# Kernel tuning notes

Hardware: AMD Instinct MI355X
Metric: run time of the kernel (lower is better)

## Reference

```python
import jax, jax.numpy as jnp
import numpy as np

E = 800000   # num edges
N = 50000    # num atoms
C = 128      # in_channels
RBF = 20     # rbf_dim
T = 1        # num_target


def setup_inputs() -> dict:
    key = jax.random.key(0)
    ks = jax.random.split(key, 12)
    return {
        "x_scalar": jax.random.normal(ks[0], (E, C), dtype=jnp.float32),
        "rbf": jax.random.normal(ks[1], (E, RBF), dtype=jnp.float32),
        "envelop_para": jax.random.uniform(ks[2], (E, 1), dtype=jnp.float32),
        "edge_index_0": jax.random.randint(ks[3], (E,), 0, N),
        "num_atoms": N,
        # learned parameters (biases initialized to zero per reset_parameters)
        "W_rbf": jax.random.normal(ks[4], (C, RBF), dtype=jnp.float32) * 0.05,
        "b_rbf": jnp.zeros((C,), dtype=jnp.float32),
        "W1": jax.random.normal(ks[5], (C, C), dtype=jnp.float32) * 0.05,
        "b1": jnp.zeros((C,), dtype=jnp.float32),
        "W2": jax.random.normal(ks[6], (C, C), dtype=jnp.float32) * 0.05,
        "b2": jnp.zeros((C,), dtype=jnp.float32),
        "W3": jax.random.normal(ks[7], (T, C), dtype=jnp.float32) * 0.05,
        "b3": jnp.zeros((T,), dtype=jnp.float32),
    }


def reference(x_scalar, rbf, envelop_para, edge_index_0, num_atoms,
              W_rbf, b_rbf, W1, b1, W2, b2, W3, b3):
    # per-edge filter: Linear(rbf) * envelope, then modulate node features
    rbf_filter = (rbf @ W_rbf.T + b_rbf) * envelop_para  # [E, C]
    msg = rbf_filter * x_scalar                           # [E, C]
    # scatter_add over destination atoms
    out = jax.ops.segment_sum(msg, edge_index_0, num_segments=num_atoms)  # [N, C]
    # small MLP head: Linear+SiLU, Linear+SiLU, Linear -> num_target
    out = jax.nn.silu(out @ W1.T + b1)
    out = jax.nn.silu(out @ W2.T + b2)
    out = out @ W3.T + b3                                 # [N, T]
    return out
```

## Files before the change

### kernel.cpp

```cpp
#include <hip/hip_runtime.h>
#include <hip/hip_bf16.h>

#define C 128
#define RBFD 20
#define NATOMS 50000
#define SCAN_CHUNK 1024
#define SLAB 128
#define SS 32

__global__ __launch_bounds__(256) void setup_kernel(
    const float* __restrict__ W1, const float* __restrict__ W2,
    float* __restrict__ W1T, float* __restrict__ W2T,
    int* __restrict__ count, float4* __restrict__ acc4,
    int n, int acc_quads)
{
    const int t = blockIdx.x * blockDim.x + threadIdx.x;
    const int stride = gridDim.x * blockDim.x;
    if (t < C * C) {
        int k = t / C;
        int c = t % C;
        W1T[t] = W1[c * C + k];
        W2T[t] = W2[c * C + k];
    }
    for (int i = t; i < n; i += stride) count[i] = 0;
    const float4 z = make_float4(0.f, 0.f, 0.f, 0.f);
    for (int i = t; i < acc_quads; i += stride) acc4[i] = z;
}

__global__ __launch_bounds__(256) void histogram_kernel(
    const int* __restrict__ idx, int* __restrict__ count, int E)
{
    int e = blockIdx.x * blockDim.x + threadIdx.x;
    if (e < E) atomicAdd(&count[idx[e]], 1);
}

__global__ __launch_bounds__(256) void scan_partials_kernel(
    const int* __restrict__ count, int* __restrict__ partial, int n)
{
    __shared__ int sm[256];
    const int start = blockIdx.x * SCAN_CHUNK;
    int s = 0;
    for (int i = threadIdx.x; i < SCAN_CHUNK; i += 256) {
        int g = start + i;
        if (g < n) s += count[g];
    }
    sm[threadIdx.x] = s;
    __syncthreads();
    for (int off = 128; off > 0; off >>= 1) {
        if (threadIdx.x < off) sm[threadIdx.x] += sm[threadIdx.x + off];
        __syncthreads();
    }
    if (threadIdx.x == 0) partial[blockIdx.x] = sm[0];
}

__global__ void scan_chunkbase_kernel(int* __restrict__ partial,
                                      int* __restrict__ base,
                                      int nchunks, int n)
{
    if (threadIdx.x == 0 && blockIdx.x == 0) {
        int run = 0;
        for (int k = 0; k < nchunks; ++k) {
            int t = partial[k];
            partial[k] = run;
            run += t;
        }
        base[n] = run;
    }
}

__global__ __launch_bounds__(1024) void scan_apply_kernel(
    const int* __restrict__ count, const int* __restrict__ chunk_base,
    int* __restrict__ base, int* __restrict__ cursor, int n)
{
    __shared__ int sm[SCAN_CHUNK];
    const int t = threadIdx.x;
    const int i = blockIdx.x * SCAN_CHUNK + t;
    int v = (i < n) ? count[i] : 0;
    sm[t] = v;
    __syncthreads();
    for (int off = 1; off < SCAN_CHUNK; off <<= 1) {
        int tmp = (t >= off) ? sm[t - off] : 0;
        __syncthreads();
        sm[t] += tmp;
        __syncthreads();
    }
    if (i < n) {
        int excl = sm[t] - v + chunk_base[blockIdx.x];
        base[i] = excl;
        cursor[i] = excl;
    }
}

__global__ __launch_bounds__(256) void fill_perm_kernel(
    const int* __restrict__ idx, int* __restrict__ cursor,
    int* __restrict__ perm, int* __restrict__ own, int E)
{
    int e = blockIdx.x * blockDim.x + threadIdx.x;
    if (e < E) {
        int a = idx[e];
        int pos = atomicAdd(&cursor[a], 1);
        perm[pos] = e;
        own[pos] = a;
    }
}

struct R5 { float4 a, b, c, d, e; };

__device__ __forceinline__ R5 load_rbf5(const float* __restrict__ rbf, int eidx) {
    const float4* q = reinterpret_cast<const float4*>(rbf + (size_t)eidx * RBFD);
    R5 r;
    r.a = q[0]; r.b = q[1]; r.c = q[2]; r.d = q[3]; r.e = q[4];
    return r;
}

__device__ __forceinline__ float dot20(const R5& p, const float* __restrict__ w,
                                       float bias) {
    float f = bias;
    f = fmaf(p.a.x, w[0],  f); f = fmaf(p.a.y, w[1],  f);
    f = fmaf(p.a.z, w[2],  f); f = fmaf(p.a.w, w[3],  f);
    f = fmaf(p.b.x, w[4],  f); f = fmaf(p.b.y, w[5],  f);
    f = fmaf(p.b.z, w[6],  f); f = fmaf(p.b.w, w[7],  f);
    f = fmaf(p.c.x, w[8],  f); f = fmaf(p.c.y, w[9],  f);
    f = fmaf(p.c.z, w[10], f); f = fmaf(p.c.w, w[11], f);
    f = fmaf(p.d.x, w[12], f); f = fmaf(p.d.y, w[13], f);
    f = fmaf(p.d.z, w[14], f); f = fmaf(p.d.w, w[15], f);
    f = fmaf(p.e.x, w[16], f); f = fmaf(p.e.y, w[17], f);
    f = fmaf(p.e.z, w[18], f); f = fmaf(p.e.w, w[19], f);
    return f;
}

__global__ __launch_bounds__(128, 2) void gather_kernel(
    const float* __restrict__ x,
    const float* __restrict__ rbf,
    const float* __restrict__ env,
    const int*   __restrict__ perm,
    const int*   __restrict__ own,
    const float* __restrict__ Wrbf,
    const float* __restrict__ brbf,
    float* __restrict__ acc)
{
    __shared__ int   e_s[SLAB];
    __shared__ float env_s[SLAB];
    __shared__ int   own_s[SLAB];

    const int tid = threadIdx.x;
    const int p0  = blockIdx.x * SLAB;

    {
        const int e = perm[p0 + tid];
        e_s[tid]   = e;
        env_s[tid] = env[e];
        own_s[tid] = own[p0 + tid];
    }

    float w[RBFD];
#pragma unroll
    for (int r = 0; r < RBFD; ++r) w[r] = Wrbf[tid * RBFD + r];
    const float bias = brbf[tid];

    __syncthreads();

    const int first_own = own_s[0];
    int   cur = first_own;
    float sum = 0.0f;

#define FLUSH()                                                                \
    do {                                                                       \
        if (cur == first_own) unsafeAtomicAdd(&acc[(size_t)cur * C + tid], sum); \
        else                  acc[(size_t)cur * C + tid] = sum;                \
    } while (0)

#pragma unroll 1
    for (int s = 0; s < SLAB; s += SS) {
        float xr[SS];
#pragma unroll
        for (int i = 0; i < SS; ++i)
            xr[i] = x[(size_t)e_s[s + i] * C + tid];
        __builtin_amdgcn_sched_barrier(0);

        R5 Pa = load_rbf5(rbf, e_s[s + 0]);
        R5 Pb = load_rbf5(rbf, e_s[s + 1]);
        __builtin_amdgcn_sched_barrier(0);

#pragma unroll
        for (int j = 0; j < SS; j += 2) {
            R5 Na, Nb;
            if (j + 2 < SS) {
                Na = load_rbf5(rbf, e_s[s + j + 2]);
                Nb = load_rbf5(rbf, e_s[s + j + 3]);
            }
            __builtin_amdgcn_sched_barrier(0);

            const float f0 = dot20(Pa, w, bias);
            const float f1 = dot20(Pb, w, bias);

            const float v0 = f0 * env_s[s + j]     * xr[j];
            const float v1 = f1 * env_s[s + j + 1] * xr[j + 1];

            const int o0 = own_s[s + j];
            const int o1 = own_s[s + j + 1];
            if (o0 != cur) { FLUSH(); sum = 0.0f; cur = o0; }
            sum += v0;
            if (o1 != cur) { FLUSH(); sum = 0.0f; cur = o1; }
            sum += v1;

            if (j + 2 < SS) { Pa = Na; Pb = Nb; }
        }
    }
    unsafeAtomicAdd(&acc[(size_t)cur * C + tid], sum);
#undef FLUSH
}

__device__ __forceinline__ float silu_f(float v) {
    return v * (1.0f / (1.0f + __expf(-v)));
}

__global__ __launch_bounds__(256) void mlp_head_kernel(
    const float* __restrict__ acc,
    const float* __restrict__ W1T,
    const float* __restrict__ b1,
    const float* __restrict__ W2T,
    const float* __restrict__ b2,
    const float* __restrict__ W3,
    const float* __restrict__ b3,
    float* __restrict__ out,
    int natoms)
{
    __shared__ float As[C][C + 1];

    const int tid = threadIdx.x;
    const int a0  = blockIdx.x * C;
    const int tc  = tid & 15;
    const int ta  = tid >> 4;
    const int abase = ta * 8;
    const int cbase = tc * 8;

    {
        const int sub = tid >> 7;
        const int k   = tid & 127;
        for (int pair = 0; pair < 64; ++pair) {
            const int al = pair * 2 + sub;
            const int a  = a0 + al;
            float v = (a < natoms) ? acc[(size_t)a * C + k] : 0.0f;
            As[k][al] = v;
        }
    }
    __syncthreads();

    float r[8][8];

#pragma unroll
    for (int i = 0; i < 8; ++i)
#pragma unroll
        for (int j = 0; j < 8; ++j) r[i][j] = 0.0f;

#pragma unroll 2
    for (int k = 0; k < C; ++k) {
        float4 bq0 = *reinterpret_cast<const float4*>(W1T + k * C + cbase);
        float4 bq1 = *reinterpret_cast<const float4*>(W1T + k * C + cbase + 4);
        float bv[8] = {bq0.x, bq0.y, bq0.z, bq0.w, bq1.x, bq1.y, bq1.z, bq1.w};
        float av[8];
#pragma unroll
        for (int i = 0; i < 8; ++i) av[i] = As[k][abase + i];
#pragma unroll
        for (int i = 0; i < 8; ++i)
#pragma unroll
            for (int j = 0; j < 8; ++j) r[i][j] = fmaf(av[i], bv[j], r[i][j]);
    }

    __syncthreads();
    {
        float bb[8];
#pragma unroll
        for (int j = 0; j < 8; ++j) bb[j] = b1[cbase + j];
#pragma unroll
        for (int i = 0; i < 8; ++i)
#pragma unroll
            for (int j = 0; j < 8; ++j)
                As[cbase + j][abase + i] = silu_f(r[i][j] + bb[j]);
    }
    __syncthreads();

#pragma unroll
    for (int i = 0; i < 8; ++i)
#pragma unroll
        for (int j = 0; j < 8; ++j) r[i][j] = 0.0f;

#pragma unroll 2
    for (int k = 0; k < C; ++k) {
        float4 bq0 = *reinterpret_cast<const float4*>(W2T + k * C + cbase);
        float4 bq1 = *reinterpret_cast<const float4*>(W2T + k * C + cbase + 4);
        float bv[8] = {bq0.x, bq0.y, bq0.z, bq0.w, bq1.x, bq1.y, bq1.z, bq1.w};
        float av[8];
#pragma unroll
        for (int i = 0; i < 8; ++i) av[i] = As[k][abase + i];
#pragma unroll
        for (int i = 0; i < 8; ++i)
#pragma unroll
            for (int j = 0; j < 8; ++j) r[i][j] = fmaf(av[i], bv[j], r[i][j]);
    }

    __syncthreads();

    {
        float bb[8], w3v[8];
#pragma unroll
        for (int j = 0; j < 8; ++j) bb[j] = b2[cbase + j];
        float4 wq0 = *reinterpret_cast<const float4*>(W3 + cbase);
        float4 wq1 = *reinterpret_cast<const float4*>(W3 + cbase + 4);
        w3v[0]=wq0.x; w3v[1]=wq0.y; w3v[2]=wq0.z; w3v[3]=wq0.w;
        w3v[4]=wq1.x; w3v[5]=wq1.y; w3v[6]=wq1.z; w3v[7]=wq1.w;

#pragma unroll
        for (int i = 0; i < 8; ++i) {
            float p = 0.0f;
#pragma unroll
            for (int j = 0; j < 8; ++j)
                p = fmaf(silu_f(r[i][j] + bb[j]), w3v[j], p);
            As[abase + i][tc] = p;
        }
    }
    __syncthreads();

    if (tid < C) {
        const int a = a0 + tid;
        if (a < natoms) {
            float s = 0.0f;
#pragma unroll
            for (int t = 0; t < 16; ++t) s += As[tid][t];
            out[a] = s + b3[0];
        }
    }
}

extern "C" void kernel_launch(void* const* d_in, const int* in_sizes, int n_in,
                              void* d_out, int out_size, void* d_ws, size_t ws_size,
                              hipStream_t stream) {
    const float* x      = (const float*)d_in[0];
    const float* rbf    = (const float*)d_in[1];
    const float* env    = (const float*)d_in[2];
    const int*   idx    = (const int*)  d_in[3];
    const float* Wrbf   = (const float*)d_in[5];
    const float* brbf   = (const float*)d_in[6];
    const float* W1     = (const float*)d_in[7];
    const float* b1     = (const float*)d_in[8];
    const float* W2     = (const float*)d_in[9];
    const float* b2     = (const float*)d_in[10];
    const float* W3     = (const float*)d_in[11];
    const float* b3     = (const float*)d_in[12];
    float*       out    = (float*)d_out;

    const int E = in_sizes[0] / C;
    const int N = NATOMS;
    const int nchunks = (N + SCAN_CHUNK - 1) / SCAN_CHUNK;

    float* acc     = (float*)d_ws;
    float* W1T     = acc + (size_t)N * C;
    float* W2T     = W1T + C * C;
    int*   count   = (int*)(W2T + C * C);
    int*   base    = count + N;
    int*   cursor  = base + (N + 1);
    int*   partial = cursor + N;
    int*   perm    = partial + 64;
    int*   own     = perm + E;

    setup_kernel<<<2048, 256, 0, stream>>>(W1, W2, W1T, W2T, count,
                                           (float4*)acc, N, (N * C) / 4);

    histogram_kernel<<<(E + 255) / 256, 256, 0, stream>>>(idx, count, E);
    scan_partials_kernel<<<nchunks, 256, 0, stream>>>(count, partial, N);
    scan_chunkbase_kernel<<<1, 64, 0, stream>>>(partial, base, nchunks, N);
    scan_apply_kernel<<<nchunks, SCAN_CHUNK, 0, stream>>>(count, partial, base, cursor, N);
    fill_perm_kernel<<<(E + 255) / 256, 256, 0, stream>>>(idx, cursor, perm, own, E);

    gather_kernel<<<E / SLAB, 128, 0, stream>>>(x, rbf, env, perm, own,
                                                Wrbf, brbf, acc);

    const int tiles = (N + C - 1) / C;
    mlp_head_kernel<<<tiles, 256, 0, stream>>>(acc, W1T, b1, W2T, b2, W3, b3, out, N);
}
```

Before: 365.9 us.

## Stage rbf rows cooperatively in LDS and double-buffer x loads across sub-slabs

Each thread used to fetch the 20-float rbf row of every edge itself, so all 128 threads of a block loaded the same data. Now the block loads each sub-slab's rbf rows once, split across threads, into a double-buffered shared array, and every thread reads the rows from LDS. The x loads for the next sub-slab are issued before computing the current one, and the sub-slab loop is fully unrolled. This cuts redundant global and L1 traffic and overlaps latency, at the cost of more registers (two xr buffers), extra LDS and a block barrier per sub-slab.

Result: faster. 330.3 us, median of 2 (-9.7%).

```diff
diff --git a/kernel.cpp b/kernel.cpp
--- a/kernel.cpp
+++ b/kernel.cpp
@@ -7,6 +7,7 @@
 #define SCAN_CHUNK 1024
 #define SLAB 128
 #define SS 32
+#define NSS (SLAB / SS)
 
 __global__ __launch_bounds__(256) void setup_kernel(
     const float* __restrict__ W1, const float* __restrict__ W2,
@@ -102,31 +103,6 @@
         perm[pos] = e;
         own[pos] = a;
     }
-}
-
-struct R5 { float4 a, b, c, d, e; };
-
-__device__ __forceinline__ R5 load_rbf5(const float* __restrict__ rbf, int eidx) {
-    const float4* q = reinterpret_cast<const float4*>(rbf + (size_t)eidx * RBFD);
-    R5 r;
-    r.a = q[0]; r.b = q[1]; r.c = q[2]; r.d = q[3]; r.e = q[4];
-    return r;
-}
-
-__device__ __forceinline__ float dot20(const R5& p, const float* __restrict__ w,
-                                       float bias) {
-    float f = bias;
-    f = fmaf(p.a.x, w[0],  f); f = fmaf(p.a.y, w[1],  f);
-    f = fmaf(p.a.z, w[2],  f); f = fmaf(p.a.w, w[3],  f);
-    f = fmaf(p.b.x, w[4],  f); f = fmaf(p.b.y, w[5],  f);
-    f = fmaf(p.b.z, w[6],  f); f = fmaf(p.b.w, w[7],  f);
-    f = fmaf(p.c.x, w[8],  f); f = fmaf(p.c.y, w[9],  f);
-    f = fmaf(p.c.z, w[10], f); f = fmaf(p.c.w, w[11], f);
-    f = fmaf(p.d.x, w[12], f); f = fmaf(p.d.y, w[13], f);
-    f = fmaf(p.d.z, w[14], f); f = fmaf(p.d.w, w[15], f);
-    f = fmaf(p.e.x, w[16], f); f = fmaf(p.e.y, w[17], f);
-    f = fmaf(p.e.z, w[18], f); f = fmaf(p.e.w, w[19], f);
-    return f;
 }
 
 __global__ __launch_bounds__(128, 2) void gather_kernel(
@@ -142,6 +118,7 @@
     __shared__ int   e_s[SLAB];
     __shared__ float env_s[SLAB];
     __shared__ int   own_s[SLAB];
+    __shared__ float rbf_s[2][SS][RBFD];
 
     const int tid = threadIdx.x;
     const int p0  = blockIdx.x * SLAB;
@@ -161,53 +138,84 @@
     __syncthreads();
 
     const int first_own = own_s[0];
-    int   cur = first_own;
+    int   cur_own = first_own;
     float sum = 0.0f;
 
 #define FLUSH()                                                                \
     do {                                                                       \
-        if (cur == first_own) unsafeAtomicAdd(&acc[(size_t)cur * C + tid], sum); \
-        else                  acc[(size_t)cur * C + tid] = sum;                \
+        if (cur_own == first_own)                                              \
+            unsafeAtomicAdd(&acc[(size_t)cur_own * C + tid], sum);             \
+        else acc[(size_t)cur_own * C + tid] = sum;                             \
     } while (0)
 
-#pragma unroll 1
-    for (int s = 0; s < SLAB; s += SS) {
-        float xr[SS];
-#pragma unroll
-        for (int i = 0; i < SS; ++i)
-            xr[i] = x[(size_t)e_s[s + i] * C + tid];
+    float xr[2][SS];
+    float st[5];
+
+#pragma unroll
+    for (int p = 0; p < 5; ++p) {
+        const int g = p * 128 + tid;
+        st[p] = rbf[(size_t)e_s[g / RBFD] * RBFD + (g % RBFD)];
+    }
+#pragma unroll
+    for (int i = 0; i < SS; ++i)
+        xr[0][i] = x[(size_t)e_s[i] * C + tid];
+    __builtin_amdgcn_sched_barrier(0);
+#pragma unroll
+    for (int p = 0; p < 5; ++p) {
+        const int g = p * 128 + tid;
+        rbf_s[0][g / RBFD][g % RBFD] = st[p];
+    }
+    __syncthreads();
+
+#pragma unroll
+    for (int ss = 0; ss < NSS; ++ss) {
+        const int sbase = ss * SS;
+        const int cur   = ss & 1;
+
+        if (ss + 1 < NSS) {
+#pragma unroll
+            for (int p = 0; p < 5; ++p) {
+                const int g = p * 128 + tid;
+                st[p] = rbf[(size_t)e_s[sbase + SS + g / RBFD] * RBFD + (g % RBFD)];
+            }
+#pragma unroll
+            for (int i = 0; i < SS; ++i)
+                xr[cur ^ 1][i] = x[(size_t)e_s[sbase + SS + i] * C + tid];
+        }
         __builtin_amdgcn_sched_barrier(0);
 
-        R5 Pa = load_rbf5(rbf, e_s[s + 0]);
-        R5 Pb = load_rbf5(rbf, e_s[s + 1]);
-        __builtin_amdgcn_sched_barrier(0);
-
-#pragma unroll
-        for (int j = 0; j < SS; j += 2) {
-            R5 Na, Nb;
-            if (j + 2 < SS) {
-                Na = load_rbf5(rbf, e_s[s + j + 2]);
-                Nb = load_rbf5(rbf, e_s[s + j + 3]);
+#pragma unroll
+        for (int j = 0; j < SS; ++j) {
+            const float4* q = reinterpret_cast<const float4*>(&rbf_s[cur][j][0]);
+            const float4 a = q[0], b = q[1], c = q[2], d = q[3], e4 = q[4];
+            float f = bias;
+            f = fmaf(a.x,  w[0],  f); f = fmaf(a.y,  w[1],  f);
+            f = fmaf(a.z,  w[2],  f); f = fmaf(a.w,  w[3],  f);
+            f = fmaf(b.x,  w[4],  f); f = fmaf(b.y,  w[5],  f);
+            f = fmaf(b.z,  w[6],  f); f = fmaf(b.w,  w[7],  f);
+            f = fmaf(c.x,  w[8],  f); f = fmaf(c.y,  w[9],  f);
+            f = fmaf(c.z,  w[10], f); f = fmaf(c.w,  w[11], f);
+            f = fmaf(d.x,  w[12], f); f = fmaf(d.y,  w[13], f);
+            f = fmaf(d.z,  w[14], f); f = fmaf(d.w,  w[15], f);
+            f = fmaf(e4.x, w[16], f); f = fmaf(e4.y, w[17], f);
+            f = fmaf(e4.z, w[18], f); f = fmaf(e4.w, w[19], f);
+
+            const float v = f * env_s[sbase + j] * xr[cur][j];
+            const int   o = own_s[sbase + j];
+            if (o != cur_own) { FLUSH(); sum = 0.0f; cur_own = o; }
+            sum += v;
+        }
+
+        if (ss + 1 < NSS) {
+#pragma unroll
+            for (int p = 0; p < 5; ++p) {
+                const int g = p * 128 + tid;
+                rbf_s[cur ^ 1][g / RBFD][g % RBFD] = st[p];
             }
-            __builtin_amdgcn_sched_barrier(0);
-
-            const float f0 = dot20(Pa, w, bias);
-            const float f1 = dot20(Pb, w, bias);
-
-            const float v0 = f0 * env_s[s + j]     * xr[j];
-            const float v1 = f1 * env_s[s + j + 1] * xr[j + 1];
-
-            const int o0 = own_s[s + j];
-            const int o1 = own_s[s + j + 1];
-            if (o0 != cur) { FLUSH(); sum = 0.0f; cur = o0; }
-            sum += v0;
-            if (o1 != cur) { FLUSH(); sum = 0.0f; cur = o1; }
-            sum += v1;
-
-            if (j + 2 < SS) { Pa = Na; Pb = Nb; }
-        }
-    }
-    unsafeAtomicAdd(&acc[(size_t)cur * C + tid], sum);
+        }
+        __syncthreads();
+    }
+    unsafeAtomicAdd(&acc[(size_t)cur_own * C + tid], sum);
 #undef FLUSH
 }
 
```

## Split gather channels across two wave blocks with rolling x prefetch ring

Applied to the files above, without the earlier changes.

The gather kernel now runs one 64-thread block per half of the channels over a 64-edge slab, replacing the 128-thread, 128-edge slab. The 32-entry register batch of x loads becomes an 8-deep rolling prefetch ring, and the owner and envelope values are packed into one int2 shared array. The aim is lower register pressure, higher occupancy and steadier overlap of loads with the rbf dot products. The cost is that both channel halves reload each edge's rbf row and the per-slab Wrbf setup. Halving the slab size also adds boundary atomics.

Measured after the change: 367.5 us. Within noise of the previous version (+0.4%).

```diff
diff --git a/kernel.cpp b/kernel.cpp
--- a/kernel.cpp
+++ b/kernel.cpp
@@ -5,8 +5,7 @@
 #define RBFD 20
 #define NATOMS 50000
 #define SCAN_CHUNK 1024
-#define SLAB 128
-#define SS 32
+#define SLAB 64
 
 __global__ __launch_bounds__(256) void setup_kernel(
     const float* __restrict__ W1, const float* __restrict__ W2,
@@ -129,7 +128,7 @@
     return f;
 }
 
-__global__ __launch_bounds__(128, 2) void gather_kernel(
+__global__ __launch_bounds__(64, 3) void gather_kernel(
     const float* __restrict__ x,
     const float* __restrict__ rbf,
     const float* __restrict__ env,
@@ -139,75 +138,80 @@
     const float* __restrict__ brbf,
     float* __restrict__ acc)
 {
-    __shared__ int   e_s[SLAB];
-    __shared__ float env_s[SLAB];
-    __shared__ int   own_s[SLAB];
-
-    const int tid = threadIdx.x;
-    const int p0  = blockIdx.x * SLAB;
+    __shared__ int  e_s[SLAB];
+    __shared__ int2 oe_s[SLAB];
+
+    const int tid  = threadIdx.x;
+    const int bid  = blockIdx.x;
+    const int slab = bid >> 1;
+    const int ch   = ((bid & 1) << 6) | tid;
+    const int p0   = slab << 6;
 
     {
         const int e = perm[p0 + tid];
-        e_s[tid]   = e;
-        env_s[tid] = env[e];
-        own_s[tid] = own[p0 + tid];
+        e_s[tid]  = e;
+        oe_s[tid] = make_int2(own[p0 + tid], __float_as_int(env[e]));
     }
 
     float w[RBFD];
 #pragma unroll
-    for (int r = 0; r < RBFD; ++r) w[r] = Wrbf[tid * RBFD + r];
-    const float bias = brbf[tid];
-
-    __syncthreads();
-
-    const int first_own = own_s[0];
-    int   cur = first_own;
+    for (int r = 0; r < RBFD; ++r) w[r] = Wrbf[ch * RBFD + r];
+    const float bias = brbf[ch];
+
+    __syncthreads();
+
+    const int first_own = oe_s[0].x;
+    int   cur_own = first_own;
     float sum = 0.0f;
 
 #define FLUSH()                                                                \
     do {                                                                       \
-        if (cur == first_own) unsafeAtomicAdd(&acc[(size_t)cur * C + tid], sum); \
-        else                  acc[(size_t)cur * C + tid] = sum;                \
+        if (cur_own == first_own)                                              \
+            unsafeAtomicAdd(&acc[(size_t)cur_own * C + ch], sum);              \
+        else acc[(size_t)cur_own * C + ch] = sum;                              \
     } while (0)
 
-#pragma unroll 1
-    for (int s = 0; s < SLAB; s += SS) {
-        float xr[SS];
-#pragma unroll
-        for (int i = 0; i < SS; ++i)
-            xr[i] = x[(size_t)e_s[s + i] * C + tid];
+    int   er[8];
+    float xp[8];
+#pragma unroll
+    for (int i = 0; i < 8; ++i) {
+        er[i] = e_s[i];
+        xp[i] = x[((size_t)er[i] << 7) + ch];
+    }
+    R5 Pa = load_rbf5(rbf, er[0]);
+    R5 Pb = load_rbf5(rbf, er[1]);
+    __builtin_amdgcn_sched_barrier(0);
+
+#pragma unroll
+    for (int j = 0; j < SLAB; j += 2) {
+        R5 Na, Nb;
+        if (j + 2 < SLAB) {
+            Na = load_rbf5(rbf, er[(j + 2) & 7]);
+            Nb = load_rbf5(rbf, er[(j + 3) & 7]);
+        }
+        int en0 = 0, en1 = 0;
+        float xn0 = 0.0f, xn1 = 0.0f;
+        if (j + 8 < SLAB) { en0 = e_s[j + 8]; xn0 = x[((size_t)en0 << 7) + ch]; }
+        if (j + 9 < SLAB) { en1 = e_s[j + 9]; xn1 = x[((size_t)en1 << 7) + ch]; }
         __builtin_amdgcn_sched_barrier(0);
 
-        R5 Pa = load_rbf5(rbf, e_s[s + 0]);
-        R5 Pb = load_rbf5(rbf, e_s[s + 1]);
-        __builtin_amdgcn_sched_barrier(0);
-
-#pragma unroll
-        for (int j = 0; j < SS; j += 2) {
-            R5 Na, Nb;
-            if (j + 2 < SS) {
-                Na = load_rbf5(rbf, e_s[s + j + 2]);
-                Nb = load_rbf5(rbf, e_s[s + j + 3]);
-            }
-            __builtin_amdgcn_sched_barrier(0);
-
-            const float f0 = dot20(Pa, w, bias);
-            const float f1 = dot20(Pb, w, bias);
-
-            const float v0 = f0 * env_s[s + j]     * xr[j];
-            const float v1 = f1 * env_s[s + j + 1] * xr[j + 1];
-
-            const int o0 = own_s[s + j];
-            const int o1 = own_s[s + j + 1];
-            if (o0 != cur) { FLUSH(); sum = 0.0f; cur = o0; }
-            sum += v0;
-            if (o1 != cur) { FLUSH(); sum = 0.0f; cur = o1; }
-            sum += v1;
-
-            if (j + 2 < SS) { Pa = Na; Pb = Nb; }
-        }
-    }
-    unsafeAtomicAdd(&acc[(size_t)cur * C + tid], sum);
+        const int2 m0 = oe_s[j];
+        const int2 m1 = oe_s[j + 1];
+        const float f0 = dot20(Pa, w, bias);
+        const float f1 = dot20(Pb, w, bias);
+        const float v0 = f0 * __int_as_float(m0.y) * xp[j & 7];
+        const float v1 = f1 * __int_as_float(m1.y) * xp[(j + 1) & 7];
+
+        if (m0.x != cur_own) { FLUSH(); sum = 0.0f; cur_own = m0.x; }
+        sum += v0;
+        if (m1.x != cur_own) { FLUSH(); sum = 0.0f; cur_own = m1.x; }
+        sum += v1;
+
+        if (j + 8 < SLAB) { er[j & 7] = en0; xp[j & 7] = xn0; }
+        if (j + 9 < SLAB) { er[(j + 1) & 7] = en1; xp[(j + 1) & 7] = xn1; }
+        Pa = Na; Pb = Nb;
+    }
+    unsafeAtomicAdd(&acc[(size_t)cur_own * C + ch], sum);
 #undef FLUSH
 }
 
@@ -373,8 +377,8 @@
     scan_apply_kernel<<<nchunks, SCAN_CHUNK, 0, stream>>>(count, partial, base, cursor, N);
     fill_perm_kernel<<<(E + 255) / 256, 256, 0, stream>>>(idx, cursor, perm, own, E);
 
-    gather_kernel<<<E / SLAB, 128, 0, stream>>>(x, rbf, env, perm, own,
-                                                Wrbf, brbf, acc);
+    gather_kernel<<<(E / SLAB) * 2, 64, 0, stream>>>(x, rbf, env, perm, own,
+                                                     Wrbf, brbf, acc);
 
     const int tiles = (N + C - 1) / C;
     mlp_head_kernel<<<tiles, 256, 0, stream>>>(acc, W1T, b1, W2T, b2, W3, b3, out, N);
```
